# Performance work log

Hardware: AMD Instinct MI355X
Metric: run time of the kernel (lower is better)

Reference implementation:

```python
import jax, jax.numpy as jnp
import numpy as np

B, C, H, W = 8, 3, 512, 512


def _spd(key, shape_prefix, c):
    a = jax.random.normal(key, shape_prefix + (c, c), dtype=jnp.float32)
    return a @ jnp.swapaxes(a, -1, -2) + jnp.eye(c, dtype=jnp.float32)


def setup_inputs() -> dict:
    key = jax.random.key(0)
    k1, k2, k3, k4, k5 = jax.random.split(key, 5)
    target = jax.random.normal(k1, (B, C, H, W), dtype=jnp.float32)
    mu = jax.random.normal(k2, (B, C, H, W), dtype=jnp.float32)
    # per-pixel covariance matrices; sigma_y must be SPD for inverse/log-det
    sigma_mu = _spd(k3, (B, H, W), C)
    sigma_n = _spd(k4, (B, H, W), C)
    sigma_y = _spd(k5, (B, H, W), C)
    return {"target": target, "mu": mu, "sigma_mu": sigma_mu,
            "sigma_n": sigma_n, "sigma_y": sigma_y}


def reference(target, mu, sigma_mu, sigma_n, sigma_y):
    # T: residual per pixel, channels-last  [B,H,W,C]
    T = jnp.transpose(target - mu, (0, 2, 3, 1))
    inv = jnp.linalg.inv(sigma_y)                      # [B,H,W,C,C] tiny 3x3 batched inverse
    # quadratic form 0.5 * T^t Sigma^{-1} T            [B,H,W]
    t1 = 0.5 * jnp.einsum('bhwc,bhwcd,bhwd->bhw', T, inv, T)
    t2 = 0.5 * jnp.log(jnp.linalg.det(sigma_y))        # [B,H,W]
    loss = jnp.mean(t1 + t2)
    # torch code zeroes loss if quadratic term blows up
    loss = jnp.where(jnp.max(t1) > 1e8, jnp.zeros_like(loss), loss)
    return loss
```

## Files before the change

kernel.cpp:

```cpp
#include <hip/hip_runtime.h>

constexpr int Bc = 8;
constexpr int Cc = 3;
constexpr int Hc = 512;
constexpr int Wc = 512;
constexpr int HW = Hc * Wc;
constexpr int NPIX = Bc * HW;


__global__ __launch_bounds__(256) void map_loss_main(
    const float* __restrict__ target,
    const float* __restrict__ mu,
    const float* __restrict__ sigma_y,
    double* __restrict__ ws_sum,
    unsigned int* __restrict__ ws_max)
{
    double local_sum = 0.0;
    float local_max = 0.0f;

    int tid = blockIdx.x * blockDim.x + threadIdx.x;
    int stride = gridDim.x * blockDim.x;

    for (int p = tid; p < NPIX; p += stride) {
        int b  = p >> 18;
        int hw = p & (HW - 1);
        int base = b * (Cc * HW) + hw;

        float t0 = target[base]            - mu[base];
        float t1 = target[base + HW]       - mu[base + HW];
        float t2 = target[base + 2 * HW]   - mu[base + 2 * HW];

        const float* s = sigma_y + (long long)p * 9;
        float s00 = s[0], s01 = s[1], s02 = s[2];
        float s11 = s[4], s12 = s[5], s22 = s[8];

        float a00 = s11 * s22 - s12 * s12;
        float a01 = s02 * s12 - s01 * s22;
        float a02 = s01 * s12 - s02 * s11;
        float a11 = s00 * s22 - s02 * s02;
        float a12 = s01 * s02 - s00 * s12;
        float a22 = s00 * s11 - s01 * s01;

        float det = s00 * a00 + s01 * a01 + s02 * a02;

        float quad = t0 * t0 * a00 + t1 * t1 * a11 + t2 * t2 * a22
                   + 2.0f * (t0 * t1 * a01 + t0 * t2 * a02 + t1 * t2 * a12);

        float t1term = 0.5f * quad / det;
        float t2term = 0.5f * logf(det);

        local_sum += (double)(t1term + t2term);
        local_max = fmaxf(local_max, t1term);
    }

    for (int off = 32; off > 0; off >>= 1) {
        local_sum += __shfl_down(local_sum, off, 64);
        local_max = fmaxf(local_max, __shfl_down(local_max, off, 64));
    }

    __shared__ double ssum[4];
    __shared__ float  smax[4];
    int wave = threadIdx.x >> 6;
    int lane = threadIdx.x & 63;
    if (lane == 0) { ssum[wave] = local_sum; smax[wave] = local_max; }
    __syncthreads();

    if (threadIdx.x == 0) {
        double bs = ssum[0] + ssum[1] + ssum[2] + ssum[3];
        float  bm = fmaxf(fmaxf(smax[0], smax[1]), fmaxf(smax[2], smax[3]));
        atomicAdd(ws_sum, bs);
        atomicMax(ws_max, __float_as_uint(bm));
    }
}

__global__ void map_loss_finalize(const double* __restrict__ ws_sum,
                                  const unsigned int* __restrict__ ws_max,
                                  float* __restrict__ out)
{
    float m = __uint_as_float(*ws_max);
    double mean = *ws_sum / (double)NPIX;
    out[0] = (m > 1e8f) ? 0.0f : (float)mean;
}

extern "C" void kernel_launch(void* const* d_in, const int* in_sizes, int n_in,
                              void* d_out, int out_size, void* d_ws, size_t ws_size,
                              hipStream_t stream) {
    const float* target  = (const float*)d_in[0];
    const float* mu      = (const float*)d_in[1];
    const float* sigma_y = (const float*)d_in[4];
    float* out = (float*)d_out;

    double*       ws_sum = (double*)d_ws;
    unsigned int* ws_max = (unsigned int*)((char*)d_ws + 8);

    hipMemsetAsync(d_ws, 0, 16, stream);

    int block = 256;
    int grid  = 2048;
    map_loss_main<<<grid, block, 0, stream>>>(target, mu, sigma_y, ws_sum, ws_max);
    map_loss_finalize<<<1, 1, 0, stream>>>(ws_sum, ws_max, out);
}
```

Before: 238.9 us.

## Stage sigma_y tiles through LDS with coalesced float4 loads, two pixels per thread

Replaces the grid-stride loop with one 512-pixel tile per block. Each block copies its slice of sigma_y into shared memory using coalesced float4 loads instead of strided 36-byte-per-thread reads, and each thread then handles two adjacent pixels with float2 loads of target and mu. The aim is better global memory coalescing on the dominant sigma_y stream. In exchange it launches 4096 blocks and issues one atomic per block, and the shared-memory reads at a stride of 18 floats per thread may cause bank conflicts.

After: 284.7 us. +19.1%, slower.

```diff
diff --git a/kernel.cpp b/kernel.cpp
--- a/kernel.cpp
+++ b/kernel.cpp
@@ -1,12 +1,14 @@
 #include <hip/hip_runtime.h>
 
-constexpr int Bc = 8;
 constexpr int Cc = 3;
 constexpr int Hc = 512;
 constexpr int Wc = 512;
 constexpr int HW = Hc * Wc;
-constexpr int NPIX = Bc * HW;
+constexpr int NPIX = 8 * HW;
 
+constexpr int TILE   = 512;
+constexpr int NBLK   = NPIX / TILE;
+constexpr int TF4    = TILE * 9 / 4;
 
 __global__ __launch_bounds__(256) void map_loss_main(
     const float* __restrict__ target,
@@ -15,22 +17,44 @@
     double* __restrict__ ws_sum,
     unsigned int* __restrict__ ws_max)
 {
+    __shared__ float4 smem[TF4];
+
+    const int t = threadIdx.x;
+    const long long tile = (long long)blockIdx.x * TILE;
+
+    const float4* s4 = (const float4*)sigma_y + (long long)blockIdx.x * TF4;
+    #pragma unroll
+    for (int j = 0; j < 4; ++j)
+        smem[j * 256 + t] = s4[j * 256 + t];
+    if (t < TF4 - 1024)
+        smem[1024 + t] = s4[1024 + t];
+    __syncthreads();
+
+    const int p0 = (int)tile + 2 * t;
+    const int b  = p0 >> 18;
+    const int hw = p0 & (HW - 1);
+    const long long base = (long long)b * (Cc * HW) + hw;
+
+    const float2* tg = (const float2*)(target + base);
+    const float2* mm = (const float2*)(mu + base);
+    float2 d0 = tg[0];        float2 m0 = mm[0];
+    float2 d1 = tg[HW / 2];   float2 m1 = mm[HW / 2];
+    float2 d2 = tg[HW];       float2 m2 = mm[HW];
+    const float T0[2] = {d0.x - m0.x, d0.y - m0.y};
+    const float T1[2] = {d1.x - m1.x, d1.y - m1.y};
+    const float T2[2] = {d2.x - m2.x, d2.y - m2.y};
+
+    const float* sp = (const float*)smem + (size_t)t * 18;
+    float S[18];
+    #pragma unroll
+    for (int k = 0; k < 18; ++k) S[k] = sp[k];
+
     double local_sum = 0.0;
-    float local_max = 0.0f;
+    float  local_max = 0.0f;
 
-    int tid = blockIdx.x * blockDim.x + threadIdx.x;
-    int stride = gridDim.x * blockDim.x;
-
-    for (int p = tid; p < NPIX; p += stride) {
-        int b  = p >> 18;
-        int hw = p & (HW - 1);
-        int base = b * (Cc * HW) + hw;
-
-        float t0 = target[base]            - mu[base];
-        float t1 = target[base + HW]       - mu[base + HW];
-        float t2 = target[base + 2 * HW]   - mu[base + 2 * HW];
-
-        const float* s = sigma_y + (long long)p * 9;
+    #pragma unroll
+    for (int i = 0; i < 2; ++i) {
+        const float* s = S + i * 9;
         float s00 = s[0], s01 = s[1], s02 = s[2];
         float s11 = s[4], s12 = s[5], s22 = s[8];
 
@@ -43,6 +67,7 @@
 
         float det = s00 * a00 + s01 * a01 + s02 * a02;
 
+        float t0 = T0[i], t1 = T1[i], t2 = T2[i];
         float quad = t0 * t0 * a00 + t1 * t1 * a11 + t2 * t2 * a22
                    + 2.0f * (t0 * t1 * a01 + t0 * t2 * a02 + t1 * t2 * a12);
 
@@ -60,12 +85,12 @@
 
     __shared__ double ssum[4];
     __shared__ float  smax[4];
-    int wave = threadIdx.x >> 6;
-    int lane = threadIdx.x & 63;
+    int wave = t >> 6;
+    int lane = t & 63;
     if (lane == 0) { ssum[wave] = local_sum; smax[wave] = local_max; }
     __syncthreads();
 
-    if (threadIdx.x == 0) {
+    if (t == 0) {
         double bs = ssum[0] + ssum[1] + ssum[2] + ssum[3];
         float  bm = fmaxf(fmaxf(smax[0], smax[1]), fmaxf(smax[2], smax[3]));
         atomicAdd(ws_sum, bs);
@@ -95,8 +120,6 @@
 
     hipMemsetAsync(d_ws, 0, 16, stream);
 
-    int block = 256;
-    int grid  = 2048;
-    map_loss_main<<<grid, block, 0, stream>>>(target, mu, sigma_y, ws_sum, ws_max);
+    map_loss_main<<<NBLK, 256, 0, stream>>>(target, mu, sigma_y, ws_sum, ws_max);
     map_loss_finalize<<<1, 1, 0, stream>>>(ws_sum, ws_max, out);
 }
```
